# Performance work log

Hardware: AMD Instinct MI355X
Metric: run time of the kernel (lower is better)

Reference implementation:

```python
import jax, jax.numpy as jnp
import numpy as np

NUM_EXPERTS = 12
TOP_K = 2
FFN_DIM = 1280
HIDDEN = 2048


def setup_inputs() -> dict:
    key = jax.random.key(0)
    k0, k1, k2, k3, k4 = jax.random.split(key, 5)
    B, S, H, F, E = 4, 1024, HIDDEN, FFN_DIM, NUM_EXPERTS
    hidden_states = jax.random.normal(k0, (B, S, H), dtype=jnp.float32)
    # single gate actually used (cluster_index_count=0 -> cluster_index_list[-1])
    gate_w = jax.random.normal(k1, (E, H), dtype=jnp.float32) * 0.02
    w1 = jax.random.normal(k2, (E, F, H), dtype=jnp.float32) * 0.02  # f1: H->F
    w2 = jax.random.normal(k3, (E, H, F), dtype=jnp.float32) * 0.02  # f2: F->H
    w3 = jax.random.normal(k4, (E, F, H), dtype=jnp.float32) * 0.02  # f3: H->F
    return {"hidden_states": hidden_states, "gate_w": gate_w, "w1": w1, "w2": w2, "w3": w3}


def reference(hidden_states, gate_w, w1, w2, w3):
    B, S, H = hidden_states.shape
    x = hidden_states.reshape(-1, H)                       # [T, H]
    T = x.shape[0]
    logits = x @ gate_w.T                                  # [T, E]
    probs = jax.nn.softmax(logits, axis=-1)
    top_w, top_i = jax.lax.top_k(probs, TOP_K)             # [T, 2]
    top_w = top_w / jnp.sum(top_w, axis=-1, keepdims=True)
    # dense combine weights [T, E]: routing weight if expert selected else 0
    cw = jnp.zeros((T, NUM_EXPERTS), dtype=x.dtype)
    cw = cw.at[jnp.arange(T)[:, None], top_i].add(top_w)
    out = jnp.zeros_like(x)
    for e in range(NUM_EXPERTS):  # fixed small expert loop
        h = jax.nn.silu(x @ w1[e].T) * (x @ w3[e].T)       # SwiGLU [T, F]
        out = out + (h @ w2[e].T) * cw[:, e:e + 1]
    return out.reshape(B, S, H)
```

## Files before the change

kernel.cpp:

```cpp
#include <hip/hip_runtime.h>
#include <hip/hip_bf16.h>

#define T_TOK 4096
#define H_DIM 2048
#define F_DIM 1280
#define NE 12
#define LDST 40

typedef float f32x4 __attribute__((ext_vector_type(4)));
typedef short bf16x8 __attribute__((ext_vector_type(8)));

__device__ __forceinline__ unsigned short f2bf(float f) {
    unsigned int u = __float_as_uint(f);
    u += 0x7FFFu + ((u >> 16) & 1u);
    return (unsigned short)(u >> 16);
}

__global__ __launch_bounds__(256) void gate_kernel(
    const float* __restrict__ x, const float* __restrict__ gw,
    int* __restrict__ counts, int* __restrict__ top_e, float* __restrict__ top_w)
{
    int gid = blockIdx.x * blockDim.x + threadIdx.x;
    int tok = gid >> 6;
    int lane = threadIdx.x & 63;
    if (tok >= T_TOK) return;
    const float* xr = x + (size_t)tok * H_DIM;
    float4 xs[8];
#pragma unroll
    for (int c = 0; c < 8; ++c) xs[c] = *(const float4*)(xr + c * 256 + lane * 4);
    float acc[NE];
#pragma unroll
    for (int e = 0; e < NE; ++e) {
        const float* gr = gw + (size_t)e * H_DIM;
        float s = 0.f;
#pragma unroll
        for (int c = 0; c < 8; ++c) {
            float4 g = *(const float4*)(gr + c * 256 + lane * 4);
            s += xs[c].x * g.x + xs[c].y * g.y + xs[c].z * g.z + xs[c].w * g.w;
        }
        acc[e] = s;
    }
#pragma unroll
    for (int e = 0; e < NE; ++e) {
#pragma unroll
        for (int off = 32; off > 0; off >>= 1)
            acc[e] += __shfl_xor(acc[e], off, 64);
    }
    if (lane == 0) {
        int b0 = 0;
#pragma unroll
        for (int e = 1; e < NE; ++e) if (acc[e] > acc[b0]) b0 = e;
        int b1 = (b0 == 0) ? 1 : 0;
#pragma unroll
        for (int e = 0; e < NE; ++e) if (e != b0 && acc[e] > acc[b1]) b1 = e;
        float t = __expf(acc[b1] - acc[b0]);
        float w0 = 1.f / (1.f + t);
        top_e[tok * 2] = b0; top_e[tok * 2 + 1] = b1;
        top_w[tok * 2] = w0; top_w[tok * 2 + 1] = 1.f - w0;
        atomicAdd(&counts[b0], 1);
        atomicAdd(&counts[b1], 1);
    }
}

__global__ void scan_kernel(const int* __restrict__ counts, int* __restrict__ offsets,
                            int* __restrict__ cursors)
{
    if (threadIdx.x == 0 && blockIdx.x == 0) {
        int s = 0;
        for (int e = 0; e < NE; ++e) { offsets[e] = s; s += counts[e]; cursors[e] = 0; }
        offsets[NE] = s;
    }
}

__global__ __launch_bounds__(256) void scatter_kernel(
    const int* __restrict__ top_e, const float* __restrict__ top_w,
    const int* __restrict__ offsets, int* __restrict__ cursors,
    int* __restrict__ row_token, float* __restrict__ row_weight)
{
    int t = blockIdx.x * blockDim.x + threadIdx.x;
    if (t >= T_TOK) return;
#pragma unroll
    for (int s = 0; s < 2; ++s) {
        int e = top_e[t * 2 + s];
        int pos = atomicAdd(&cursors[e], 1);
        int r = offsets[e] + pos;
        row_token[r] = t;
        row_weight[r] = top_w[t * 2 + s];
    }
}

__global__ __launch_bounds__(256) void ffn1_kernel(
    const float* __restrict__ x, const float* __restrict__ w1, const float* __restrict__ w3,
    const int* __restrict__ counts, const int* __restrict__ offsets,
    const int* __restrict__ row_token, unsigned short* __restrict__ hbuf)
{
    int e = blockIdx.z;
    int cnt = counts[e];
    int m0 = blockIdx.y * 64;
    if (m0 >= cnt) return;
    int base = offsets[e];
    int n0 = blockIdx.x * 64;

    __shared__ unsigned short As[64 * LDST];
    __shared__ unsigned short B1s[64 * LDST];
    __shared__ unsigned short B3s[64 * LDST];

    int t = threadIdx.x;
    int lane = t & 63;
    int wid = t >> 6;
    int wm = wid >> 1, wn = wid & 1;
    int lr = lane & 15, lq = lane >> 4;

    int sr = t >> 2;
    int sc = (t & 3) * 8;

    int arow_valid = (m0 + sr) < cnt;
    int tokenRow = arow_valid ? row_token[base + m0 + sr] : 0;
    const float* aP  = x  + (size_t)tokenRow * H_DIM + sc;
    const float* b1P = w1 + ((size_t)e * F_DIM + (n0 + sr)) * H_DIM + sc;
    const float* b3P = w3 + ((size_t)e * F_DIM + (n0 + sr)) * H_DIM + sc;

    f32x4 acc1[2][2] = {{{0.f,0.f,0.f,0.f},{0.f,0.f,0.f,0.f}},{{0.f,0.f,0.f,0.f},{0.f,0.f,0.f,0.f}}};
    f32x4 acc3[2][2] = {{{0.f,0.f,0.f,0.f},{0.f,0.f,0.f,0.f}},{{0.f,0.f,0.f,0.f},{0.f,0.f,0.f,0.f}}};

    for (int k0 = 0; k0 < H_DIM; k0 += 32) {
        float4 a0, a1;
        if (arow_valid) { a0 = *(const float4*)(aP + k0); a1 = *(const float4*)(aP + k0 + 4); }
        else            { a0 = make_float4(0, 0, 0, 0);   a1 = a0; }
        float4 p0 = *(const float4*)(b1P + k0); float4 p1 = *(const float4*)(b1P + k0 + 4);
        float4 q0 = *(const float4*)(b3P + k0); float4 q1 = *(const float4*)(b3P + k0 + 4);
        unsigned short* d = As + sr * LDST + sc;
        d[0]=f2bf(a0.x); d[1]=f2bf(a0.y); d[2]=f2bf(a0.z); d[3]=f2bf(a0.w);
        d[4]=f2bf(a1.x); d[5]=f2bf(a1.y); d[6]=f2bf(a1.z); d[7]=f2bf(a1.w);
        d = B1s + sr * LDST + sc;
        d[0]=f2bf(p0.x); d[1]=f2bf(p0.y); d[2]=f2bf(p0.z); d[3]=f2bf(p0.w);
        d[4]=f2bf(p1.x); d[5]=f2bf(p1.y); d[6]=f2bf(p1.z); d[7]=f2bf(p1.w);
        d = B3s + sr * LDST + sc;
        d[0]=f2bf(q0.x); d[1]=f2bf(q0.y); d[2]=f2bf(q0.z); d[3]=f2bf(q0.w);
        d[4]=f2bf(q1.x); d[5]=f2bf(q1.y); d[6]=f2bf(q1.z); d[7]=f2bf(q1.w);
        __syncthreads();

        bf16x8 af[2], b1f[2], b3f[2];
#pragma unroll
        for (int ms = 0; ms < 2; ++ms)
            af[ms] = *(bf16x8*)(As + (wm * 32 + ms * 16 + lr) * LDST + lq * 8);
#pragma unroll
        for (int ns = 0; ns < 2; ++ns) {
            b1f[ns] = *(bf16x8*)(B1s + (wn * 32 + ns * 16 + lr) * LDST + lq * 8);
            b3f[ns] = *(bf16x8*)(B3s + (wn * 32 + ns * 16 + lr) * LDST + lq * 8);
        }
#pragma unroll
        for (int ms = 0; ms < 2; ++ms)
#pragma unroll
            for (int ns = 0; ns < 2; ++ns) {
                acc1[ms][ns] = __builtin_amdgcn_mfma_f32_16x16x32_bf16(af[ms], b1f[ns], acc1[ms][ns], 0, 0, 0);
                acc3[ms][ns] = __builtin_amdgcn_mfma_f32_16x16x32_bf16(af[ms], b3f[ns], acc3[ms][ns], 0, 0, 0);
            }
        __syncthreads();
    }

#pragma unroll
    for (int ms = 0; ms < 2; ++ms) {
        int r0 = wm * 32 + ms * 16 + lq * 4;
#pragma unroll
        for (int ns = 0; ns < 2; ++ns) {
            int c = n0 + wn * 32 + ns * 16 + lr;
#pragma unroll
            for (int i = 0; i < 4; ++i) {
                int r = r0 + i;
                if (m0 + r < cnt) {
                    float a = acc1[ms][ns][i];
                    float hv = (a / (1.f + __expf(-a))) * acc3[ms][ns][i];
                    hbuf[(size_t)(base + m0 + r) * F_DIM + c] = f2bf(hv);
                }
            }
        }
    }
}

__global__ __launch_bounds__(256) void ffn2_kernel(
    const unsigned short* __restrict__ hbuf, const float* __restrict__ w2,
    const int* __restrict__ counts, const int* __restrict__ offsets,
    const int* __restrict__ row_token, const float* __restrict__ row_weight,
    float* __restrict__ out)
{
    int e = blockIdx.z;
    int cnt = counts[e];
    int m0 = blockIdx.y * 64;
    if (m0 >= cnt) return;
    int base = offsets[e];
    int n0 = blockIdx.x * 64;

    __shared__ unsigned short As[64 * LDST];
    __shared__ unsigned short Bs[64 * LDST];

    int t = threadIdx.x;
    int lane = t & 63;
    int wid = t >> 6;
    int wm = wid >> 1, wn = wid & 1;
    int lr = lane & 15, lq = lane >> 4;

    int sr = t >> 2;
    int sc = (t & 3) * 8;

    int arow_valid = (m0 + sr) < cnt;
    const unsigned short* aP = hbuf + (size_t)(base + m0 + (arow_valid ? sr : 0)) * F_DIM + sc;
    const float* bP = w2 + ((size_t)e * H_DIM + (n0 + sr)) * F_DIM + sc;

    f32x4 acc[2][2] = {{{0.f,0.f,0.f,0.f},{0.f,0.f,0.f,0.f}},{{0.f,0.f,0.f,0.f},{0.f,0.f,0.f,0.f}}};

    for (int k0 = 0; k0 < F_DIM; k0 += 32) {
        uint4 av = make_uint4(0, 0, 0, 0);
        if (arow_valid) av = *(const uint4*)(aP + k0);
        float4 p0 = *(const float4*)(bP + k0); float4 p1 = *(const float4*)(bP + k0 + 4);
        *(uint4*)(As + sr * LDST + sc) = av;
        unsigned short* d = Bs + sr * LDST + sc;
        d[0]=f2bf(p0.x); d[1]=f2bf(p0.y); d[2]=f2bf(p0.z); d[3]=f2bf(p0.w);
        d[4]=f2bf(p1.x); d[5]=f2bf(p1.y); d[6]=f2bf(p1.z); d[7]=f2bf(p1.w);
        __syncthreads();

        bf16x8 af[2], bf[2];
#pragma unroll
        for (int ms = 0; ms < 2; ++ms)
            af[ms] = *(bf16x8*)(As + (wm * 32 + ms * 16 + lr) * LDST + lq * 8);
#pragma unroll
        for (int ns = 0; ns < 2; ++ns)
            bf[ns] = *(bf16x8*)(Bs + (wn * 32 + ns * 16 + lr) * LDST + lq * 8);
#pragma unroll
        for (int ms = 0; ms < 2; ++ms)
#pragma unroll
            for (int ns = 0; ns < 2; ++ns)
                acc[ms][ns] = __builtin_amdgcn_mfma_f32_16x16x32_bf16(af[ms], bf[ns], acc[ms][ns], 0, 0, 0);
        __syncthreads();
    }

#pragma unroll
    for (int ms = 0; ms < 2; ++ms) {
        int r0 = wm * 32 + ms * 16 + lq * 4;
#pragma unroll
        for (int i = 0; i < 4; ++i) {
            int r = r0 + i;
            if (m0 + r < cnt) {
                int token = row_token[base + m0 + r];
                float wgt = row_weight[base + m0 + r];
#pragma unroll
                for (int ns = 0; ns < 2; ++ns) {
                    int c = n0 + wn * 32 + ns * 16 + lr;
                    atomicAdd(&out[(size_t)token * H_DIM + c], acc[ms][ns][i] * wgt);
                }
            }
        }
    }
}

extern "C" void kernel_launch(void* const* d_in, const int* in_sizes, int n_in,
                              void* d_out, int out_size, void* d_ws, size_t ws_size,
                              hipStream_t stream)
{
    const float* x  = (const float*)d_in[0];
    const float* gw = (const float*)d_in[1];
    const float* w1 = (const float*)d_in[2];
    const float* w2 = (const float*)d_in[3];
    const float* w3 = (const float*)d_in[4];
    float* out = (float*)d_out;

    int* wsI = (int*)d_ws;
    int* counts  = wsI;
    int* cursors = wsI + 16;
    int* offsets = wsI + 32;
    int* top_e   = wsI + 64;
    int* row_token = top_e + 2 * T_TOK;
    float* top_w     = (float*)(row_token + 2 * T_TOK);
    float* row_weight = top_w + 2 * T_TOK;
    unsigned short* hbuf = (unsigned short*)(row_weight + 2 * T_TOK);

    hipMemsetAsync(counts, 0, 64 * sizeof(int), stream);
    hipMemsetAsync(out, 0, (size_t)out_size * sizeof(float), stream);

    gate_kernel<<<T_TOK / 4, 256, 0, stream>>>(x, gw, counts, top_e, top_w);
    scan_kernel<<<1, 64, 0, stream>>>(counts, offsets, cursors);
    scatter_kernel<<<T_TOK / 256, 256, 0, stream>>>(top_e, top_w, offsets, cursors,
                                                    row_token, row_weight);
    dim3 g1(F_DIM / 64, 64, NE);
    ffn1_kernel<<<g1, 256, 0, stream>>>(x, w1, w3, counts, offsets, row_token, hbuf);
    dim3 g2(H_DIM / 64, 64, NE);
    ffn2_kernel<<<g2, 256, 0, stream>>>(hbuf, w2, counts, offsets, row_token, row_weight, out);
}
```

Baseline: 920.3 us.

## Pre-convert to bf16, use direct global-to-LDS loads, larger tiles, atomic-free combine

Adds conversion kernels that turn activations and all expert weights into bf16 once per call, so the FFN GEMMs load bf16 directly into shared memory with global_load_lds. Both expert GEMMs move to 128x128 tiles with a 4x4 MFMA grid per wave for more reuse. The atomic scatter into the output is replaced by a per-row ybuf plus a combine kernel indexed by inverse positions. This adds per-call conversion traffic over all weights and drops the LDS padding, which may cause bank conflicts.

```diff
diff --git a/kernel.cpp b/kernel.cpp
--- a/kernel.cpp
+++ b/kernel.cpp
@@ -1,11 +1,10 @@
 #include <hip/hip_runtime.h>
-#include <hip/hip_bf16.h>
 
 #define T_TOK 4096
 #define H_DIM 2048
 #define F_DIM 1280
 #define NE 12
-#define LDST 40
+#define TOTAL_ROWS (2 * T_TOK)
 
 typedef float f32x4 __attribute__((ext_vector_type(4)));
 typedef short bf16x8 __attribute__((ext_vector_type(8)));
@@ -14,6 +13,25 @@
     unsigned int u = __float_as_uint(f);
     u += 0x7FFFu + ((u >> 16) & 1u);
     return (unsigned short)(u >> 16);
+}
+
+__device__ __forceinline__ void gl2lds16(const void* g, void* l) {
+    __builtin_amdgcn_global_load_lds(
+        (const __attribute__((address_space(1))) unsigned int*)g,
+        (__attribute__((address_space(3))) unsigned int*)l,
+        16, 0, 0);
+}
+
+__global__ __launch_bounds__(256) void convert_kernel(
+    const float* __restrict__ src, unsigned short* __restrict__ dst)
+{
+    size_t i = ((size_t)blockIdx.x * 256 + threadIdx.x) * 8;
+    float4 a = *(const float4*)(src + i);
+    float4 b = *(const float4*)(src + i + 4);
+    unsigned short o[8];
+    o[0] = f2bf(a.x); o[1] = f2bf(a.y); o[2] = f2bf(a.z); o[3] = f2bf(a.w);
+    o[4] = f2bf(b.x); o[5] = f2bf(b.y); o[6] = f2bf(b.z); o[7] = f2bf(b.w);
+    *(uint4*)(dst + i) = *(const uint4*)o;
 }
 
 __global__ __launch_bounds__(256) void gate_kernel(
@@ -75,7 +93,8 @@
 __global__ __launch_bounds__(256) void scatter_kernel(
     const int* __restrict__ top_e, const float* __restrict__ top_w,
     const int* __restrict__ offsets, int* __restrict__ cursors,
-    int* __restrict__ row_token, float* __restrict__ row_weight)
+    int* __restrict__ row_token, float* __restrict__ row_weight,
+    int* __restrict__ inv_pos)
 {
     int t = blockIdx.x * blockDim.x + threadIdx.x;
     if (t >= T_TOK) return;
@@ -86,24 +105,26 @@
         int r = offsets[e] + pos;
         row_token[r] = t;
         row_weight[r] = top_w[t * 2 + s];
+        inv_pos[t * 2 + s] = r;
     }
 }
 
 __global__ __launch_bounds__(256) void ffn1_kernel(
-    const float* __restrict__ x, const float* __restrict__ w1, const float* __restrict__ w3,
+    const unsigned short* __restrict__ xb, const unsigned short* __restrict__ w1b,
+    const unsigned short* __restrict__ w3b,
     const int* __restrict__ counts, const int* __restrict__ offsets,
     const int* __restrict__ row_token, unsigned short* __restrict__ hbuf)
 {
     int e = blockIdx.z;
     int cnt = counts[e];
-    int m0 = blockIdx.y * 64;
+    int m0 = blockIdx.y * 128;
     if (m0 >= cnt) return;
     int base = offsets[e];
-    int n0 = blockIdx.x * 64;
-
-    __shared__ unsigned short As[64 * LDST];
-    __shared__ unsigned short B1s[64 * LDST];
-    __shared__ unsigned short B3s[64 * LDST];
+    int n0 = blockIdx.x * 128;
+
+    __shared__ unsigned short As[128 * 32];
+    __shared__ unsigned short B1s[128 * 32];
+    __shared__ unsigned short B3s[128 * 32];
 
     int t = threadIdx.x;
     int lane = t & 63;
@@ -111,67 +132,65 @@
     int wm = wid >> 1, wn = wid & 1;
     int lr = lane & 15, lq = lane >> 4;
 
-    int sr = t >> 2;
-    int sc = (t & 3) * 8;
-
-    int arow_valid = (m0 + sr) < cnt;
-    int tokenRow = arow_valid ? row_token[base + m0 + sr] : 0;
-    const float* aP  = x  + (size_t)tokenRow * H_DIM + sc;
-    const float* b1P = w1 + ((size_t)e * F_DIM + (n0 + sr)) * H_DIM + sc;
-    const float* b3P = w3 + ((size_t)e * F_DIM + (n0 + sr)) * H_DIM + sc;
-
-    f32x4 acc1[2][2] = {{{0.f,0.f,0.f,0.f},{0.f,0.f,0.f,0.f}},{{0.f,0.f,0.f,0.f},{0.f,0.f,0.f,0.f}}};
-    f32x4 acc3[2][2] = {{{0.f,0.f,0.f,0.f},{0.f,0.f,0.f,0.f}},{{0.f,0.f,0.f,0.f},{0.f,0.f,0.f,0.f}}};
+    int srow = t >> 2;
+    int chunk = t & 3;
+    int tok0 = row_token[base + min(m0 + srow, cnt - 1)];
+    int tok1 = row_token[base + min(m0 + 64 + srow, cnt - 1)];
+    const unsigned short* gA0 = xb + (size_t)tok0 * H_DIM + chunk * 8;
+    const unsigned short* gA1 = xb + (size_t)tok1 * H_DIM + chunk * 8;
+    const unsigned short* gB1 = w1b + ((size_t)e * F_DIM + n0 + srow) * H_DIM + chunk * 8;
+    const unsigned short* gB3 = w3b + ((size_t)e * F_DIM + n0 + srow) * H_DIM + chunk * 8;
+    const size_t rowskip = (size_t)64 * H_DIM;
+
+    unsigned short* lA0 = As + wid * 512;
+    unsigned short* lA1 = As + 2048 + wid * 512;
+    unsigned short* lB10 = B1s + wid * 512;
+    unsigned short* lB11 = B1s + 2048 + wid * 512;
+    unsigned short* lB30 = B3s + wid * 512;
+    unsigned short* lB31 = B3s + 2048 + wid * 512;
+
+    f32x4 acc1[4][4] = {};
+    f32x4 acc3[4][4] = {};
 
     for (int k0 = 0; k0 < H_DIM; k0 += 32) {
-        float4 a0, a1;
-        if (arow_valid) { a0 = *(const float4*)(aP + k0); a1 = *(const float4*)(aP + k0 + 4); }
-        else            { a0 = make_float4(0, 0, 0, 0);   a1 = a0; }
-        float4 p0 = *(const float4*)(b1P + k0); float4 p1 = *(const float4*)(b1P + k0 + 4);
-        float4 q0 = *(const float4*)(b3P + k0); float4 q1 = *(const float4*)(b3P + k0 + 4);
-        unsigned short* d = As + sr * LDST + sc;
-        d[0]=f2bf(a0.x); d[1]=f2bf(a0.y); d[2]=f2bf(a0.z); d[3]=f2bf(a0.w);
-        d[4]=f2bf(a1.x); d[5]=f2bf(a1.y); d[6]=f2bf(a1.z); d[7]=f2bf(a1.w);
-        d = B1s + sr * LDST + sc;
-        d[0]=f2bf(p0.x); d[1]=f2bf(p0.y); d[2]=f2bf(p0.z); d[3]=f2bf(p0.w);
-        d[4]=f2bf(p1.x); d[5]=f2bf(p1.y); d[6]=f2bf(p1.z); d[7]=f2bf(p1.w);
-        d = B3s + sr * LDST + sc;
-        d[0]=f2bf(q0.x); d[1]=f2bf(q0.y); d[2]=f2bf(q0.z); d[3]=f2bf(q0.w);
-        d[4]=f2bf(q1.x); d[5]=f2bf(q1.y); d[6]=f2bf(q1.z); d[7]=f2bf(q1.w);
+        gl2lds16(gA0 + k0, lA0);
+        gl2lds16(gA1 + k0, lA1);
+        gl2lds16(gB1 + k0, lB10);
+        gl2lds16(gB1 + rowskip + k0, lB11);
+        gl2lds16(gB3 + k0, lB30);
+        gl2lds16(gB3 + rowskip + k0, lB31);
         __syncthreads();
 
-        bf16x8 af[2], b1f[2], b3f[2];
-#pragma unroll
-        for (int ms = 0; ms < 2; ++ms)
-            af[ms] = *(bf16x8*)(As + (wm * 32 + ms * 16 + lr) * LDST + lq * 8);
-#pragma unroll
-        for (int ns = 0; ns < 2; ++ns) {
-            b1f[ns] = *(bf16x8*)(B1s + (wn * 32 + ns * 16 + lr) * LDST + lq * 8);
-            b3f[ns] = *(bf16x8*)(B3s + (wn * 32 + ns * 16 + lr) * LDST + lq * 8);
-        }
-#pragma unroll
-        for (int ms = 0; ms < 2; ++ms)
-#pragma unroll
-            for (int ns = 0; ns < 2; ++ns) {
-                acc1[ms][ns] = __builtin_amdgcn_mfma_f32_16x16x32_bf16(af[ms], b1f[ns], acc1[ms][ns], 0, 0, 0);
-                acc3[ms][ns] = __builtin_amdgcn_mfma_f32_16x16x32_bf16(af[ms], b3f[ns], acc3[ms][ns], 0, 0, 0);
+        bf16x8 af[4];
+#pragma unroll
+        for (int ms = 0; ms < 4; ++ms)
+            af[ms] = *(const bf16x8*)(As + (wm * 64 + ms * 16 + lr) * 32 + lq * 8);
+#pragma unroll
+        for (int ns = 0; ns < 4; ++ns) {
+            bf16x8 b1 = *(const bf16x8*)(B1s + (wn * 64 + ns * 16 + lr) * 32 + lq * 8);
+            bf16x8 b3 = *(const bf16x8*)(B3s + (wn * 64 + ns * 16 + lr) * 32 + lq * 8);
+#pragma unroll
+            for (int ms = 0; ms < 4; ++ms) {
+                acc1[ms][ns] = __builtin_amdgcn_mfma_f32_16x16x32_bf16(af[ms], b1, acc1[ms][ns], 0, 0, 0);
+                acc3[ms][ns] = __builtin_amdgcn_mfma_f32_16x16x32_bf16(af[ms], b3, acc3[ms][ns], 0, 0, 0);
             }
+        }
         __syncthreads();
     }
 
 #pragma unroll
-    for (int ms = 0; ms < 2; ++ms) {
-        int r0 = wm * 32 + ms * 16 + lq * 4;
-#pragma unroll
-        for (int ns = 0; ns < 2; ++ns) {
-            int c = n0 + wn * 32 + ns * 16 + lr;
-#pragma unroll
-            for (int i = 0; i < 4; ++i) {
-                int r = r0 + i;
-                if (m0 + r < cnt) {
+    for (int ms = 0; ms < 4; ++ms) {
+#pragma unroll
+        for (int i = 0; i < 4; ++i) {
+            int r = wm * 64 + ms * 16 + lq * 4 + i;
+            if (m0 + r < cnt) {
+                size_t rowoff = (size_t)(base + m0 + r) * F_DIM;
+#pragma unroll
+                for (int ns = 0; ns < 4; ++ns) {
+                    int c = n0 + wn * 64 + ns * 16 + lr;
                     float a = acc1[ms][ns][i];
                     float hv = (a / (1.f + __expf(-a))) * acc3[ms][ns][i];
-                    hbuf[(size_t)(base + m0 + r) * F_DIM + c] = f2bf(hv);
+                    hbuf[rowoff + c] = f2bf(hv);
                 }
             }
         }
@@ -179,20 +198,19 @@
 }
 
 __global__ __launch_bounds__(256) void ffn2_kernel(
-    const unsigned short* __restrict__ hbuf, const float* __restrict__ w2,
+    const unsigned short* __restrict__ hbuf, const unsigned short* __restrict__ w2b,
     const int* __restrict__ counts, const int* __restrict__ offsets,
-    const int* __restrict__ row_token, const float* __restrict__ row_weight,
-    float* __restrict__ out)
+    const float* __restrict__ row_weight, float* __restrict__ ybuf)
 {
     int e = blockIdx.z;
     int cnt = counts[e];
-    int m0 = blockIdx.y * 64;
+    int m0 = blockIdx.y * 128;
     if (m0 >= cnt) return;
     int base = offsets[e];
-    int n0 = blockIdx.x * 64;
-
-    __shared__ unsigned short As[64 * LDST];
-    __shared__ unsigned short Bs[64 * LDST];
+    int n0 = blockIdx.x * 128;
+
+    __shared__ unsigned short As[128 * 32];
+    __shared__ unsigned short Bs[128 * 32];
 
     int t = threadIdx.x;
     int lane = t & 63;
@@ -200,56 +218,75 @@
     int wm = wid >> 1, wn = wid & 1;
     int lr = lane & 15, lq = lane >> 4;
 
-    int sr = t >> 2;
-    int sc = (t & 3) * 8;
-
-    int arow_valid = (m0 + sr) < cnt;
-    const unsigned short* aP = hbuf + (size_t)(base + m0 + (arow_valid ? sr : 0)) * F_DIM + sc;
-    const float* bP = w2 + ((size_t)e * H_DIM + (n0 + sr)) * F_DIM + sc;
-
-    f32x4 acc[2][2] = {{{0.f,0.f,0.f,0.f},{0.f,0.f,0.f,0.f}},{{0.f,0.f,0.f,0.f},{0.f,0.f,0.f,0.f}}};
+    int srow = t >> 2;
+    int chunk = t & 3;
+    const unsigned short* gA0 = hbuf + (size_t)(base + min(m0 + srow, cnt - 1)) * F_DIM + chunk * 8;
+    const unsigned short* gA1 = hbuf + (size_t)(base + min(m0 + 64 + srow, cnt - 1)) * F_DIM + chunk * 8;
+    const unsigned short* gB = w2b + ((size_t)e * H_DIM + n0 + srow) * F_DIM + chunk * 8;
+    const size_t rowskip = (size_t)64 * F_DIM;
+
+    unsigned short* lA0 = As + wid * 512;
+    unsigned short* lA1 = As + 2048 + wid * 512;
+    unsigned short* lB0 = Bs + wid * 512;
+    unsigned short* lB1 = Bs + 2048 + wid * 512;
+
+    f32x4 acc[4][4] = {};
 
     for (int k0 = 0; k0 < F_DIM; k0 += 32) {
-        uint4 av = make_uint4(0, 0, 0, 0);
-        if (arow_valid) av = *(const uint4*)(aP + k0);
-        float4 p0 = *(const float4*)(bP + k0); float4 p1 = *(const float4*)(bP + k0 + 4);
-        *(uint4*)(As + sr * LDST + sc) = av;
-        unsigned short* d = Bs + sr * LDST + sc;
-        d[0]=f2bf(p0.x); d[1]=f2bf(p0.y); d[2]=f2bf(p0.z); d[3]=f2bf(p0.w);
-        d[4]=f2bf(p1.x); d[5]=f2bf(p1.y); d[6]=f2bf(p1.z); d[7]=f2bf(p1.w);
+        gl2lds16(gA0 + k0, lA0);
+        gl2lds16(gA1 + k0, lA1);
+        gl2lds16(gB + k0, lB0);
+        gl2lds16(gB + rowskip + k0, lB1);
         __syncthreads();
 
-        bf16x8 af[2], bf[2];
-#pragma unroll
-        for (int ms = 0; ms < 2; ++ms)
-            af[ms] = *(bf16x8*)(As + (wm * 32 + ms * 16 + lr) * LDST + lq * 8);
-#pragma unroll
-        for (int ns = 0; ns < 2; ++ns)
-            bf[ns] = *(bf16x8*)(Bs + (wn * 32 + ns * 16 + lr) * LDST + lq * 8);
-#pragma unroll
-        for (int ms = 0; ms < 2; ++ms)
-#pragma unroll
-            for (int ns = 0; ns < 2; ++ns)
-                acc[ms][ns] = __builtin_amdgcn_mfma_f32_16x16x32_bf16(af[ms], bf[ns], acc[ms][ns], 0, 0, 0);
+        bf16x8 af[4];
+#pragma unroll
+        for (int ms = 0; ms < 4; ++ms)
+            af[ms] = *(const bf16x8*)(As + (wm * 64 + ms * 16 + lr) * 32 + lq * 8);
+#pragma unroll
+        for (int ns = 0; ns < 4; ++ns) {
+            bf16x8 b = *(const bf16x8*)(Bs + (wn * 64 + ns * 16 + lr) * 32 + lq * 8);
+#pragma unroll
+            for (int ms = 0; ms < 4; ++ms)
+                acc[ms][ns] = __builtin_amdgcn_mfma_f32_16x16x32_bf16(af[ms], b, acc[ms][ns], 0, 0, 0);
+        }
         __syncthreads();
     }
 
 #pragma unroll
-    for (int ms = 0; ms < 2; ++ms) {
-        int r0 = wm * 32 + ms * 16 + lq * 4;
+    for (int ms = 0; ms < 4; ++ms) {
 #pragma unroll
         for (int i = 0; i < 4; ++i) {
-            int r = r0 + i;
+            int r = wm * 64 + ms * 16 + lq * 4 + i;
             if (m0 + r < cnt) {
-                int token = row_token[base + m0 + r];
                 float wgt = row_weight[base + m0 + r];
-#pragma unroll
-                for (int ns = 0; ns < 2; ++ns) {
-                    int c = n0 + wn * 32 + ns * 16 + lr;
-                    atomicAdd(&out[(size_t)token * H_DIM + c], acc[ms][ns][i] * wgt);
+                size_t rowoff = (size_t)(base + m0 + r) * H_DIM;
+#pragma unroll
+                for (int ns = 0; ns < 4; ++ns) {
+                    int c = n0 + wn * 64 + ns * 16 + lr;
+                    ybuf[rowoff + c] = acc[ms][ns][i] * wgt;
                 }
             }
         }
+    }
+}
+
+__global__ __launch_bounds__(256) void combine_kernel(
+    const float* __restrict__ ybuf, const int* __restrict__ inv_pos,
+    float* __restrict__ out)
+{
+    int tk = blockIdx.x;
+    int p0 = inv_pos[2 * tk];
+    int p1 = inv_pos[2 * tk + 1];
+    const float4* y0 = (const float4*)(ybuf + (size_t)p0 * H_DIM);
+    const float4* y1 = (const float4*)(ybuf + (size_t)p1 * H_DIM);
+    float4* o = (float4*)(out + (size_t)tk * H_DIM);
+#pragma unroll
+    for (int i = threadIdx.x; i < H_DIM / 4; i += 256) {
+        float4 a = y0[i], b = y1[i];
+        float4 r;
+        r.x = a.x + b.x; r.y = a.y + b.y; r.z = a.z + b.z; r.w = a.w + b.w;
+        o[i] = r;
     }
 }
 
@@ -264,25 +301,39 @@
     const float* w3 = (const float*)d_in[4];
     float* out = (float*)d_out;
 
-    int* wsI = (int*)d_ws;
-    int* counts  = wsI;
-    int* cursors = wsI + 16;
-    int* offsets = wsI + 32;
-    int* top_e   = wsI + 64;
-    int* row_token = top_e + 2 * T_TOK;
-    float* top_w     = (float*)(row_token + 2 * T_TOK);
-    float* row_weight = top_w + 2 * T_TOK;
-    unsigned short* hbuf = (unsigned short*)(row_weight + 2 * T_TOK);
+    unsigned char* p = (unsigned char*)d_ws;
+    int* counts     = (int*)p;  p += 256;
+    int* cursors    = (int*)p;  p += 256;
+    int* offsets    = (int*)p;  p += 256;
+    int* top_e      = (int*)p;  p += 2 * T_TOK * 4;
+    float* top_w    = (float*)p; p += 2 * T_TOK * 4;
+    int* row_token  = (int*)p;  p += 2 * T_TOK * 4;
+    float* row_weight = (float*)p; p += 2 * T_TOK * 4;
+    int* inv_pos    = (int*)p;  p += 2 * T_TOK * 4;
+    unsigned short* xb  = (unsigned short*)p; p += (size_t)T_TOK * H_DIM * 2;
+    unsigned short* w2b = (unsigned short*)p; p += (size_t)NE * H_DIM * F_DIM * 2;
+    unsigned short* hb  = (unsigned short*)p; p += (size_t)TOTAL_ROWS * F_DIM * 2;
+    unsigned short* w1b = (unsigned short*)p;
+    unsigned short* w3b = (unsigned short*)(p + (size_t)NE * F_DIM * H_DIM * 2);
+    float* ybuf = (float*)p;
+
+    const int WELEM = NE * F_DIM * H_DIM;
+    convert_kernel<<<T_TOK * H_DIM / 2048, 256, 0, stream>>>(x, xb);
+    convert_kernel<<<WELEM / 2048, 256, 0, stream>>>(w1, w1b);
+    convert_kernel<<<WELEM / 2048, 256, 0, stream>>>(w2, w2b);
+    convert_kernel<<<WELEM / 2048, 256, 0, stream>>>(w3, w3b);
 
     hipMemsetAsync(counts, 0, 64 * sizeof(int), stream);
-    hipMemsetAsync(out, 0, (size_t)out_size * sizeof(float), stream);
-
     gate_kernel<<<T_TOK / 4, 256, 0, stream>>>(x, gw, counts, top_e, top_w);
     scan_kernel<<<1, 64, 0, stream>>>(counts, offsets, cursors);
     scatter_kernel<<<T_TOK / 256, 256, 0, stream>>>(top_e, top_w, offsets, cursors,
-                                                    row_token, row_weight);
-    dim3 g1(F_DIM / 64, 64, NE);
-    ffn1_kernel<<<g1, 256, 0, stream>>>(x, w1, w3, counts, offsets, row_token, hbuf);
-    dim3 g2(H_DIM / 64, 64, NE);
-    ffn2_kernel<<<g2, 256, 0, stream>>>(hbuf, w2, counts, offsets, row_token, row_weight, out);
-}
+                                                    row_token, row_weight, inv_pos);
+
+    dim3 g1(F_DIM / 128, 32, NE);
+    ffn1_kernel<<<g1, 256, 0, stream>>>(xb, w1b, w3b, counts, offsets, row_token, hb);
+
+    dim3 g2(H_DIM / 128, 32, NE);
+    ffn2_kernel<<<g2, 256, 0, stream>>>(hb, w2b, counts, offsets, row_weight, ybuf);
+
+    combine_kernel<<<T_TOK, 256, 0, stream>>>(ybuf, inv_pos, out);
+}
```

Measured after the change: 839.8 us. -8.7%, faster.
